# Optimization experiments

Hardware: AMD Instinct MI355X
Metric: run time of the kernel (lower is better)

Reference implementation:

```python
import jax, jax.numpy as jnp
import numpy as np

B, S, NGB, NG, DIM = 64, 4096, 13, 48, 3
NCH = [8, 8, 1]
NSHELLS = 8


def setup_inputs() -> dict:
    key = jax.random.key(0)
    ks = jax.random.split(key, 16)
    rng = np.random.default_rng(0)
    # valid row-wise permutations of the N_ngb neighbor slots per group op
    GnnPerms = jnp.asarray(np.argsort(rng.random((NG, NGB)), axis=1), dtype=jnp.int64)
    NNSites = jax.random.randint(ks[0], (NGB, S), 0, S, dtype=jnp.int64)
    SitesToShells = jax.random.randint(ks[1], (S,), 0, NSHELLS, dtype=jnp.int64)
    # block-diagonal (Ng*dim, Ng*dim) cartesian rotation blocks
    blk = rng.normal(size=(NG, DIM, DIM)).astype(np.float32) * 0.5
    gd = np.zeros((NG * DIM, NG * DIM), np.float32)
    for g in range(NG):
        gd[g * DIM:(g + 1) * DIM, g * DIM:(g + 1) * DIM] = blk[g]
    gdiags = jnp.asarray(gd)
    std = 0.2
    return {
        "InStates": jax.random.normal(ks[2], (B, 1, S), jnp.float32),
        "Psi0": jax.random.normal(ks[3], (NCH[0], 1, NGB), jnp.float32) * std,
        "bias0": jax.random.normal(ks[4], (NCH[0], 1), jnp.float32) * std,
        "Psi1": jax.random.normal(ks[5], (NCH[1], NCH[0], NGB), jnp.float32) * std,
        "bias1": jax.random.normal(ks[6], (NCH[1], 1), jnp.float32) * std,
        "Psi2": jax.random.normal(ks[7], (NCH[2], NCH[1], NGB), jnp.float32) * std,
        "bias2": jax.random.normal(ks[8], (NCH[2], 1), jnp.float32) * std,
        "wtVC": jax.random.normal(ks[9], (DIM, NGB), jnp.float32) * std,
        "ShellWeights": jax.random.normal(ks[10], (NSHELLS,), jnp.float32) * std,
        "gdiags": gdiags,
        "GnnPerms": GnnPerms,
        "NNSites": NNSites,
        "SitesToShells": SitesToShells,
    }


def _rearrange(x, NNSites):
    # x: (B, Nch, S) -> (B, Nch*N_ngb, S); subchannel j of channel c holds x[b, c, NNSites[j, s]]
    b, c, s = x.shape
    return x[:, :, NNSites].reshape(b, c * NGB, s)


def _gconv(x, W, b):
    # x: (B, NchIn*N_ngb, S); W: (NchOut, NchIn, N_ngb); b: (NchOut, 1)
    # group-rotated weights: GW[o, g, c*N_ngb+j] = W[o, c, GnnPerms[g, j]]
    GW = _gconv.GW_cache  # set per-call below via closure-free pattern; replaced in reference
    raise NotImplementedError


def reference(InStates, Psi0, bias0, Psi1, bias1, Psi2, bias2, wtVC,
              ShellWeights, gdiags, GnnPerms, NNSites, SitesToShells):
    act = jax.nn.softplus

    def gconv(x, W, b):
        # rotated weights: (NchOut, Ng, NchIn*N_ngb)
        GW = W[:, :, GnnPerms].transpose(0, 2, 1, 3).reshape(W.shape[0], NG, -1)
        h = jnp.einsum('ogk,bks->bogs', GW, x) + b[:, :, None]  # (B, NchOut, Ng, S)
        return act(h).mean(axis=2)                               # group-orbit average

    out = _rearrange(InStates, NNSites)
    for W, b in ((Psi0, bias0), (Psi1, bias1), (Psi2, bias2)):
        out = gconv(out, W, b)                 # (B, NchOut, S)
        out = _rearrange(out, NNSites)         # (B, NchOut*N_ngb, S)
    # vector channel: row g*dim+d of P is wtVC[d, GnnPerms[g]]
    P = wtVC[:, GnnPerms].transpose(1, 0, 2).reshape(NG * DIM, NGB)
    Wvc = gdiags @ P                           # (Ng*dim, N_ngb)
    v = jnp.einsum('kn,bns->bks', Wvc, out)    # (B, Ng*dim, S)
    v = v.reshape(-1, NG, DIM, out.shape[-1]).mean(axis=1)  # (B, dim, S)
    v = v * ShellWeights[SitesToShells]        # per-site shell weighting
    return v.sum(axis=2) / out.shape[-1]       # (B, dim)
```

## Files before the change

### kernel.cpp

```cpp
#include <hip/hip_runtime.h>
#include <hip/hip_bf16.h>

#define BATCH 64
#define SITES 4096
#define NGB 13
#define NGRP 48
#define SDIM 3

typedef __bf16 bf16x8 __attribute__((ext_vector_type(8)));
typedef float  f32x4  __attribute__((ext_vector_type(4)));

#define OFF_AVC  0
#define OFF_U    64
#define OFF_A0   67648
#define OFF_A1   2164800
#define OFF_PART 4261952
#define UW0H 0
#define UW0L 12288
#define UW1H 24576
#define UW1L 73728
#define UW2H 122880
#define UW2L 129024

__device__ __forceinline__ float softplus_f(float h) {
    return fmaxf(h, 0.f) + __logf(1.f + __expf(-fabsf(h)));
}

__global__ __launch_bounds__(256) void precompute_kernel(
    const float* __restrict__ Psi0, const float* __restrict__ Psi1,
    const float* __restrict__ Psi2, const float* __restrict__ wtVC,
    const float* __restrict__ gdiags, const int* __restrict__ perms,
    float* __restrict__ ws)
{
    float*  Avc = ws + OFF_AVC;
    __bf16* U   = (__bf16*)(ws + OFF_U);
    int t = blockIdx.x * 256 + threadIdx.x;
    if (t < 12288) {
        int k = t & 31, row = t >> 5;
        int o = row / NGRP, g = row - o * NGRP;
        float w = (k < NGB) ? Psi0[o * NGB + perms[g * NGB + k]] : 0.f;
        __bf16 hi = (__bf16)w;
        U[UW0H + t] = hi;
        U[UW0L + t] = (__bf16)(w - (float)hi);
    } else if (t < 61440) {
        int u = t - 12288;
        int k = u & 127, row = u >> 7;
        int o = row / NGRP, g = row - o * NGRP;
        float w = 0.f;
        if (k < 104) { int j = k >> 3, c = k & 7;
                       w = Psi1[(o * 8 + c) * NGB + perms[g * NGB + j]]; }
        __bf16 hi = (__bf16)w;
        U[UW1H + u] = hi;
        U[UW1L + u] = (__bf16)(w - (float)hi);
    } else if (t < 67584) {
        int u = t - 61440;
        int k = u & 127, g = u >> 7;
        float w = 0.f;
        if (k < 104) { int j = k >> 3, c = k & 7;
                       w = Psi2[c * NGB + perms[g * NGB + j]]; }
        __bf16 hi = (__bf16)w;
        U[UW2H + u] = hi;
        U[UW2L + u] = (__bf16)(w - (float)hi);
    } else if (t < 67584 + 39 * NGRP) {
        int t2 = t - 67584;
        int g = t2 % NGRP, u = t2 / NGRP;
        int d = u / NGB, n = u % NGB;
        const int row = g * SDIM + d;
        float s = 0.f;
        for (int k = 0; k < NGRP * SDIM; k++) {
            int g2 = k / SDIM, d2 = k - g2 * SDIM;
            float p = wtVC[d2 * NGB + perms[g2 * NGB + n]];
            s = fmaf(gdiags[row * (NGRP * SDIM) + k], p, s);
        }
        atomicAdd(&Avc[u], s * (1.f / 48.f));
    }
}

template<int NCIN, int NCTOT, int CT, int KPAD, int KSTR, int NWAVES, int NWN,
         int CHUNKS>
__global__ __launch_bounds__(NWAVES * 64) void layer_mfma(
    const float* __restrict__ prev,
    const __bf16* __restrict__ Wh,
    const __bf16* __restrict__ Wl,
    const float* __restrict__ bias,
    const int*   __restrict__ NN,
    float* __restrict__ out)
{
    constexpr int NTHR   = NWAVES * 64;
    constexpr int M      = NCTOT * NGRP;
    constexpr int MTILES = M / 16, NTILES = CT / 16;
    constexpr int NWM    = NWAVES / NWN;
    constexpr int MT_W   = MTILES / NWM, NT_W = NTILES / NWN;
    constexpr int KT     = KPAD / 32;
    constexpr int GS     = NGB * CT;
    constexpr int SPT    = (GS + NTHR - 1) / NTHR;
    constexpr int CPB    = SITES / CT;
    constexpr int BUF    = CT * KSTR;
    constexpr int BPB    = CPB / CHUNKS;

    static_assert(MT_W * 16 == NGRP, "wave covers exactly one o");
    static_assert(NWM * MT_W == MTILES && NWN * NT_W == NTILES, "");
    static_assert((KPAD & 31) == 0 && (KSTR & 7) == 0, "");
    static_assert(CPB % CHUNKS == 0, "block stays within one batch");

    __shared__ __bf16 xh_lds[2 * BUF];
    __shared__ __bf16 xl_lds[2 * BUF];

    const int tid  = threadIdx.x;
    const int wave = tid >> 6, lane = tid & 63;
    const int m16  = lane & 15, quad = lane >> 4;

    const int bid    = blockIdx.x;
    const int b      = bid / BPB;
    const int octet  = bid % BPB;
    const int s0base = octet * (CHUNKS * CT);

    int sj[SPT], scol[SPT];
    bool sv[SPT];
#pragma unroll
    for (int i = 0; i < SPT; i++) {
        int site = tid + i * NTHR;
        sv[i] = (site < GS);
        int ss = sv[i] ? site : 0;
        sj[i] = ss / CT;
        scol[i] = ss % CT;
    }

    auto stage_site = [&](int i, int nn, __bf16* dh, __bf16* dl) {
        if constexpr (NCIN == 1) {
            float v = prev[(size_t)b * SITES + nn];
            __bf16 hi = (__bf16)v;
            dh[scol[i] * KSTR + sj[i]] = hi;
            dl[scol[i] * KSTR + sj[i]] = (__bf16)(v - (float)hi);
        } else {
            const float4* p4 = (const float4*)(prev + ((size_t)(b * SITES + nn)) * 8);
            float4 u0 = p4[0], u1 = p4[1];
            float v[8] = {u0.x, u0.y, u0.z, u0.w, u1.x, u1.y, u1.z, u1.w};
            bf16x8 hv, lv;
#pragma unroll
            for (int c8 = 0; c8 < 8; c8++) {
                __bf16 hi = (__bf16)v[c8];
                hv[c8] = hi;
                lv[c8] = (__bf16)(v[c8] - (float)hi);
            }
            *(bf16x8*)(dh + scol[i] * KSTR + sj[i] * 8) = hv;
            *(bf16x8*)(dl + scol[i] * KSTR + sj[i] * 8) = lv;
        }
    };

    if constexpr (NCIN == 1) {
        for (int e = tid; e < 2 * CT * (KPAD - NGB); e += NTHR) {
            int buf = e / (CT * (KPAD - NGB));
            int r   = e % (CT * (KPAD - NGB));
            int col = r / (KPAD - NGB), p = r % (KPAD - NGB);
            xh_lds[buf * BUF + col * KSTR + NGB + p] = (__bf16)0.f;
            xl_lds[buf * BUF + col * KSTR + NGB + p] = (__bf16)0.f;
        }
    } else {
        const bf16x8 z8 = {};
        for (int e = tid; e < 2 * CT * 3; e += NTHR) {
            int buf = e / (CT * 3);
            int r   = e % (CT * 3);
            int col = r % CT, z = r / CT;
            *(bf16x8*)(xh_lds + buf * BUF + col * KSTR + 104 + z * 8) = z8;
            *(bf16x8*)(xl_lds + buf * BUF + col * KSTR + 104 + z * 8) = z8;
        }
    }

#pragma unroll
    for (int i = 0; i < SPT; i++) if (sv[i]) {
        int nn = NN[sj[i] * SITES + s0base + scol[i]];
        stage_site(i, nn, xh_lds, xl_lds);
    }
    int nnA[SPT];
    if (CHUNKS > 1) {
        const int s1 = s0base + CT;
#pragma unroll
        for (int i = 0; i < SPT; i++)
            nnA[i] = sv[i] ? NN[sj[i] * SITES + s1 + scol[i]] : 0;
    }
    __syncthreads();

    const int wave_mt0 = (wave / NWN) * MT_W;
    const int wave_nt0 = (wave % NWN) * NT_W;
    const int o_g      = (wave_mt0 * 16) / NGRP;
    const float bo     = bias[o_g];

#pragma unroll 1
    for (int c = 0; c < CHUNKS; c++) {
        const int cur = c & 1;
        const __bf16* xh = xh_lds + cur * BUF;
        const __bf16* xl = xl_lds + cur * BUF;

        f32x4 acc[MT_W][NT_W];
#pragma unroll
        for (int mt = 0; mt < MT_W; mt++)
#pragma unroll
            for (int nt = 0; nt < NT_W; nt++) acc[mt][nt] = (f32x4){0.f, 0.f, 0.f, 0.f};

#pragma unroll
        for (int kt = 0; kt < KT; kt++) {
            const int koff = kt * 32 + quad * 8;
            bf16x8 ah[MT_W], al[MT_W], bh[NT_W], bl[NT_W];
#pragma unroll
            for (int mt = 0; mt < MT_W; mt++) {
                int row = (wave_mt0 + mt) * 16 + m16;
                ah[mt] = *(const bf16x8*)(Wh + (size_t)row * KPAD + koff);
                al[mt] = *(const bf16x8*)(Wl + (size_t)row * KPAD + koff);
            }
#pragma unroll
            for (int nt = 0; nt < NT_W; nt++) {
                int cbase = ((wave_nt0 + nt) * 16 + m16) * KSTR + koff;
                bh[nt] = *(const bf16x8*)(xh + cbase);
                bl[nt] = *(const bf16x8*)(xl + cbase);
            }
#pragma unroll
            for (int mt = 0; mt < MT_W; mt++)
#pragma unroll
                for (int nt = 0; nt < NT_W; nt++)
                    acc[mt][nt] = __builtin_amdgcn_mfma_f32_16x16x32_bf16(
                        ah[mt], bh[nt], acc[mt][nt], 0, 0, 0);
#pragma unroll
            for (int mt = 0; mt < MT_W; mt++)
#pragma unroll
                for (int nt = 0; nt < NT_W; nt++)
                    acc[mt][nt] = __builtin_amdgcn_mfma_f32_16x16x32_bf16(
                        al[mt], bh[nt], acc[mt][nt], 0, 0, 0);
#pragma unroll
            for (int mt = 0; mt < MT_W; mt++)
#pragma unroll
                for (int nt = 0; nt < NT_W; nt++)
                    acc[mt][nt] = __builtin_amdgcn_mfma_f32_16x16x32_bf16(
                        ah[mt], bl[nt], acc[mt][nt], 0, 0, 0);
        }

        const int s0c = s0base + c * CT;
#pragma unroll
        for (int nt = 0; nt < NT_W; nt++) {
            float s = 0.f;
#pragma unroll
            for (int mt = 0; mt < MT_W; mt++)
#pragma unroll
                for (int r = 0; r < 4; r++)
                    s += softplus_f(acc[mt][nt][r] + bo);
            s += __shfl_xor(s, 16);
            s += __shfl_xor(s, 32);
            if (quad == 0)
                out[((size_t)(b * SITES + s0c + (wave_nt0 + nt) * 16 + m16)) * NCTOT + o_g]
                    = s * (1.f / 48.f);
        }

        if (c + 1 < CHUNKS) {
            __bf16* dh = xh_lds + (cur ^ 1) * BUF;
            __bf16* dl = xl_lds + (cur ^ 1) * BUF;
#pragma unroll
            for (int i = 0; i < SPT; i++) if (sv[i])
                stage_site(i, nnA[i], dh, dl);
            if (c + 2 < CHUNKS) {
                const int s2 = s0base + (c + 2) * CT;
#pragma unroll
                for (int i = 0; i < SPT; i++)
                    nnA[i] = sv[i] ? NN[sj[i] * SITES + s2 + scol[i]] : 0;
            }
        }
        __syncthreads();
    }
}

__global__ __launch_bounds__(256) void reduce_a(
    const float* __restrict__ A2, const int* __restrict__ NN,
    const int* __restrict__ s2sh, const float* __restrict__ sw,
    const float* __restrict__ Avc, float* __restrict__ partial)
{
    const int b = blockIdx.x >> 4;
    const int chunk = blockIdx.x & 15;
    const int tid = threadIdx.x;
    const int s = (chunk << 8) + tid;
    const float* a = A2 + (size_t)b * SITES;

    float y0 = 0.f, y1 = 0.f, y2 = 0.f;
#pragma unroll
    for (int n = 0; n < NGB; n++) {
        float v = a[NN[n * SITES + s]];
        y0 = fmaf(Avc[n],           v, y0);
        y1 = fmaf(Avc[NGB + n],     v, y1);
        y2 = fmaf(Avc[2 * NGB + n], v, y2);
    }
    const float wgt = sw[s2sh[s]];
    y0 *= wgt; y1 *= wgt; y2 *= wgt;

    __shared__ float red[3][256];
    red[0][tid] = y0; red[1][tid] = y1; red[2][tid] = y2;
    __syncthreads();
    for (int st = 128; st > 0; st >>= 1) {
        if (tid < st) {
            red[0][tid] += red[0][tid + st];
            red[1][tid] += red[1][tid + st];
            red[2][tid] += red[2][tid + st];
        }
        __syncthreads();
    }
    if (tid < 3) partial[(b * 16 + chunk) * 3 + tid] = red[tid][0];
}

__global__ __launch_bounds__(256) void reduce_b(
    const float* __restrict__ partial, float* __restrict__ out)
{
    int t = threadIdx.x;
    if (t < BATCH * 3) {
        int b = t / 3, d = t - b * 3;
        float s = 0.f;
        for (int c = 0; c < 16; c++) s += partial[(b * 16 + c) * 3 + d];
        out[t] = s * (1.f / (float)SITES);
    }
}

extern "C" void kernel_launch(void* const* d_in, const int* in_sizes, int n_in,
                              void* d_out, int out_size, void* d_ws, size_t ws_size,
                              hipStream_t stream)
{
    const float* InStates = (const float*)d_in[0];
    const float* Psi0     = (const float*)d_in[1];
    const float* bias0    = (const float*)d_in[2];
    const float* Psi1     = (const float*)d_in[3];
    const float* bias1    = (const float*)d_in[4];
    const float* Psi2     = (const float*)d_in[5];
    const float* bias2    = (const float*)d_in[6];
    const float* wtVC     = (const float*)d_in[7];
    const float* ShellW   = (const float*)d_in[8];
    const float* gdiags   = (const float*)d_in[9];
    const int*   GnnPerms = (const int*)d_in[10];
    const int*   NNSites  = (const int*)d_in[11];
    const int*   S2Sh     = (const int*)d_in[12];

    float*  ws   = (float*)d_ws;
    float*  Avc  = ws + OFF_AVC;
    __bf16* U    = (__bf16*)(ws + OFF_U);
    float*  A0   = ws + OFF_A0;
    float*  A1   = ws + OFF_A1;
    float*  A2   = ws + OFF_A0;
    float*  PART = ws + OFF_PART;

    float* out = (float*)d_out;

    hipMemsetAsync(Avc, 0, 64 * sizeof(float), stream);
    precompute_kernel<<<272, 256, 0, stream>>>(Psi0, Psi1, Psi2, wtVC, gdiags,
                                               GnnPerms, ws);

    constexpr int CHUNKS = 8;
    constexpr int NBLK   = BATCH * (SITES / 64) / CHUNKS;

    layer_mfma<1, 8, 64, 32, 40, 8, 1, CHUNKS><<<NBLK, 512, 0, stream>>>(
        InStates, U + UW0H, U + UW0L, bias0, NNSites, A0);
    layer_mfma<8, 8, 64, 128, 136, 8, 1, CHUNKS><<<NBLK, 512, 0, stream>>>(
        A0, U + UW1H, U + UW1L, bias1, NNSites, A1);
    layer_mfma<8, 1, 64, 128, 136, 4, 4, CHUNKS><<<NBLK, 256, 0, stream>>>(
        A1, U + UW2H, U + UW2L, bias2, NNSites, A2);

    reduce_a<<<BATCH * 16, 256, 0, stream>>>(A2, NNSites, S2Sh, ShellW, Avc, PART);
    reduce_b<<<1, 256, 0, stream>>>(PART, out);
}
```

Measured before the change: 331.5 us.

## Store intermediate activations as bf16 hi/lo pairs and stage gathers via direct-to-LDS loads

```diff
diff --git a/kernel.cpp b/kernel.cpp
--- a/kernel.cpp
+++ b/kernel.cpp
@@ -12,8 +12,10 @@
 
 #define OFF_AVC  0
 #define OFF_U    64
-#define OFF_A0   67648
-#define OFF_A1   2164800
+#define OFF_A0H  67648
+#define OFF_A0L  1116224
+#define OFF_A1H  2164800
+#define OFF_A1L  3213376
 #define OFF_PART 4261952
 #define UW0H 0
 #define UW0L 12288
@@ -24,6 +26,13 @@
 
 __device__ __forceinline__ float softplus_f(float h) {
     return fmaxf(h, 0.f) + __logf(1.f + __expf(-fabsf(h)));
+}
+
+__device__ __forceinline__ void gld_lds16(const __bf16* g, __bf16* l) {
+    __builtin_amdgcn_global_load_lds(
+        (const __attribute__((address_space(1))) void*)g,
+        (__attribute__((address_space(3))) void*)l,
+        16, 0, 0);
 }
 
 __global__ __launch_bounds__(256) void precompute_kernel(
@@ -76,15 +85,19 @@
     }
 }
 
-template<int NCIN, int NCTOT, int CT, int KPAD, int KSTR, int NWAVES, int NWN,
-         int CHUNKS>
+template<int NCIN, int NCTOT, int OUTF32, int CT, int KPAD, int KSTR,
+         int NWAVES, int NWN, int CHUNKS>
 __global__ __launch_bounds__(NWAVES * 64) void layer_mfma(
-    const float* __restrict__ prev,
+    const float*  __restrict__ prevF,
+    const __bf16* __restrict__ prevH,
+    const __bf16* __restrict__ prevL,
     const __bf16* __restrict__ Wh,
     const __bf16* __restrict__ Wl,
-    const float* __restrict__ bias,
-    const int*   __restrict__ NN,
-    float* __restrict__ out)
+    const float*  __restrict__ bias,
+    const int*    __restrict__ NN,
+    float*  __restrict__ outF,
+    __bf16* __restrict__ outH,
+    __bf16* __restrict__ outL)
 {
     constexpr int NTHR   = NWAVES * 64;
     constexpr int M      = NCTOT * NGRP;
@@ -92,16 +105,17 @@
     constexpr int NWM    = NWAVES / NWN;
     constexpr int MT_W   = MTILES / NWM, NT_W = NTILES / NWN;
     constexpr int KT     = KPAD / 32;
+    constexpr int CPB    = SITES / CT;
+    constexpr int BPB    = CPB / CHUNKS;
+    constexpr int BUF    = (NCIN == 1) ? CT * KSTR : 16 * CT * 8;
     constexpr int GS     = NGB * CT;
     constexpr int SPT    = (GS + NTHR - 1) / NTHR;
-    constexpr int CPB    = SITES / CT;
-    constexpr int BUF    = CT * KSTR;
-    constexpr int BPB    = CPB / CHUNKS;
+    constexpr int JPW    = (NGB + NWAVES - 1) / NWAVES;
 
     static_assert(MT_W * 16 == NGRP, "wave covers exactly one o");
     static_assert(NWM * MT_W == MTILES && NWN * NT_W == NTILES, "");
-    static_assert((KPAD & 31) == 0 && (KSTR & 7) == 0, "");
     static_assert(CPB % CHUNKS == 0, "block stays within one batch");
+    static_assert(NCIN == 1 || CT == 64, "DMA staging: lane==col");
 
     __shared__ __bf16 xh_lds[2 * BUF];
     __shared__ __bf16 xl_lds[2 * BUF];
@@ -125,27 +139,11 @@
         sj[i] = ss / CT;
         scol[i] = ss % CT;
     }
-
-    auto stage_site = [&](int i, int nn, __bf16* dh, __bf16* dl) {
-        if constexpr (NCIN == 1) {
-            float v = prev[(size_t)b * SITES + nn];
-            __bf16 hi = (__bf16)v;
-            dh[scol[i] * KSTR + sj[i]] = hi;
-            dl[scol[i] * KSTR + sj[i]] = (__bf16)(v - (float)hi);
-        } else {
-            const float4* p4 = (const float4*)(prev + ((size_t)(b * SITES + nn)) * 8);
-            float4 u0 = p4[0], u1 = p4[1];
-            float v[8] = {u0.x, u0.y, u0.z, u0.w, u1.x, u1.y, u1.z, u1.w};
-            bf16x8 hv, lv;
-#pragma unroll
-            for (int c8 = 0; c8 < 8; c8++) {
-                __bf16 hi = (__bf16)v[c8];
-                hv[c8] = hi;
-                lv[c8] = (__bf16)(v[c8] - (float)hi);
-            }
-            *(bf16x8*)(dh + scol[i] * KSTR + sj[i] * 8) = hv;
-            *(bf16x8*)(dl + scol[i] * KSTR + sj[i] * 8) = lv;
-        }
+    auto stage_site1 = [&](int i, int nn, __bf16* dh, __bf16* dl) {
+        float v = prevF[(size_t)b * SITES + nn];
+        __bf16 hi = (__bf16)v;
+        dh[scol[i] * KSTR + sj[i]] = hi;
+        dl[scol[i] * KSTR + sj[i]] = (__bf16)(v - (float)hi);
     };
 
     if constexpr (NCIN == 1) {
@@ -158,26 +156,44 @@
         }
     } else {
         const bf16x8 z8 = {};
-        for (int e = tid; e < 2 * CT * 3; e += NTHR) {
-            int buf = e / (CT * 3);
-            int r   = e % (CT * 3);
-            int col = r % CT, z = r / CT;
-            *(bf16x8*)(xh_lds + buf * BUF + col * KSTR + 104 + z * 8) = z8;
-            *(bf16x8*)(xl_lds + buf * BUF + col * KSTR + 104 + z * 8) = z8;
-        }
-    }
-
-#pragma unroll
-    for (int i = 0; i < SPT; i++) if (sv[i]) {
-        int nn = NN[sj[i] * SITES + s0base + scol[i]];
-        stage_site(i, nn, xh_lds, xl_lds);
-    }
+        for (int e = tid; e < 2 * 3 * CT; e += NTHR) {
+            int buf = e / (3 * CT), r = e % (3 * CT);
+            *(bf16x8*)(xh_lds + buf * BUF + (13 * CT + r) * 8) = z8;
+            *(bf16x8*)(xl_lds + buf * BUF + (13 * CT + r) * 8) = z8;
+        }
+    }
+
     int nnA[SPT];
-    if (CHUNKS > 1) {
-        const int s1 = s0base + CT;
-#pragma unroll
-        for (int i = 0; i < SPT; i++)
-            nnA[i] = sv[i] ? NN[sj[i] * SITES + s1 + scol[i]] : 0;
+    int nnP[JPW];
+    if constexpr (NCIN == 1) {
+#pragma unroll
+        for (int i = 0; i < SPT; i++) if (sv[i]) {
+            int nn = NN[sj[i] * SITES + s0base + scol[i]];
+            stage_site1(i, nn, xh_lds, xl_lds);
+        }
+        if (CHUNKS > 1) {
+            const int s1 = s0base + CT;
+#pragma unroll
+            for (int i = 0; i < SPT; i++)
+                nnA[i] = sv[i] ? NN[sj[i] * SITES + s1 + scol[i]] : 0;
+        }
+    } else {
+#pragma unroll
+        for (int u = 0; u < JPW; u++) {
+            int jj = wave + u * NWAVES;
+            if (jj < NGB) {
+                int nn0 = NN[jj * SITES + s0base + lane];
+                gld_lds16(prevH + ((size_t)(b * SITES + nn0)) * 8, xh_lds + jj * CT * 8);
+                gld_lds16(prevL + ((size_t)(b * SITES + nn0)) * 8, xl_lds + jj * CT * 8);
+            }
+        }
+        if (CHUNKS > 1) {
+#pragma unroll
+            for (int u = 0; u < JPW; u++) {
+                int jj = wave + u * NWAVES;
+                nnP[u] = (jj < NGB) ? NN[jj * SITES + s0base + CT + lane] : 0;
+            }
+        }
     }
     __syncthreads();
 
@@ -189,6 +205,30 @@
 #pragma unroll 1
     for (int c = 0; c < CHUNKS; c++) {
         const int cur = c & 1;
+
+        if constexpr (NCIN == 8) {
+            if (c + 1 < CHUNKS) {
+                __bf16* dh = xh_lds + (cur ^ 1) * BUF;
+                __bf16* dl = xl_lds + (cur ^ 1) * BUF;
+#pragma unroll
+                for (int u = 0; u < JPW; u++) {
+                    int jj = wave + u * NWAVES;
+                    if (jj < NGB) {
+                        gld_lds16(prevH + ((size_t)(b * SITES + nnP[u])) * 8, dh + jj * CT * 8);
+                        gld_lds16(prevL + ((size_t)(b * SITES + nnP[u])) * 8, dl + jj * CT * 8);
+                    }
+                }
+                if (c + 2 < CHUNKS) {
+                    const int s2 = s0base + (c + 2) * CT;
+#pragma unroll
+                    for (int u = 0; u < JPW; u++) {
+                        int jj = wave + u * NWAVES;
+                        nnP[u] = (jj < NGB) ? NN[jj * SITES + s2 + lane] : 0;
+                    }
+                }
+            }
+        }
+
         const __bf16* xh = xh_lds + cur * BUF;
         const __bf16* xl = xl_lds + cur * BUF;
 
@@ -210,7 +250,11 @@
             }
 #pragma unroll
             for (int nt = 0; nt < NT_W; nt++) {
-                int cbase = ((wave_nt0 + nt) * 16 + m16) * KSTR + koff;
+                int cbase;
+                if constexpr (NCIN == 1)
+                    cbase = ((wave_nt0 + nt) * 16 + m16) * KSTR + koff;
+                else
+                    cbase = ((kt * 4 + quad) * CT + (wave_nt0 + nt) * 16 + m16) * 8;
                 bh[nt] = *(const bf16x8*)(xh + cbase);
                 bl[nt] = *(const bf16x8*)(xl + cbase);
             }
@@ -245,22 +289,32 @@
                     s += softplus_f(acc[mt][nt][r] + bo);
             s += __shfl_xor(s, 16);
             s += __shfl_xor(s, 32);
-            if (quad == 0)
-                out[((size_t)(b * SITES + s0c + (wave_nt0 + nt) * 16 + m16)) * NCTOT + o_g]
-                    = s * (1.f / 48.f);
-        }
-
-        if (c + 1 < CHUNKS) {
-            __bf16* dh = xh_lds + (cur ^ 1) * BUF;
-            __bf16* dl = xl_lds + (cur ^ 1) * BUF;
-#pragma unroll
-            for (int i = 0; i < SPT; i++) if (sv[i])
-                stage_site(i, nnA[i], dh, dl);
-            if (c + 2 < CHUNKS) {
-                const int s2 = s0base + (c + 2) * CT;
-#pragma unroll
-                for (int i = 0; i < SPT; i++)
-                    nnA[i] = sv[i] ? NN[sj[i] * SITES + s2 + scol[i]] : 0;
+            if (quad == 0) {
+                float sv2 = s * (1.f / 48.f);
+                size_t idx = (size_t)(b * SITES + s0c + (wave_nt0 + nt) * 16 + m16);
+                if constexpr (OUTF32) {
+                    outF[idx] = sv2;
+                } else {
+                    __bf16 hi = (__bf16)sv2;
+                    outH[idx * NCTOT + o_g] = hi;
+                    outL[idx * NCTOT + o_g] = (__bf16)(sv2 - (float)hi);
+                }
+            }
+        }
+
+        if constexpr (NCIN == 1) {
+            if (c + 1 < CHUNKS) {
+                __bf16* dh = xh_lds + (cur ^ 1) * BUF;
+                __bf16* dl = xl_lds + (cur ^ 1) * BUF;
+#pragma unroll
+                for (int i = 0; i < SPT; i++) if (sv[i])
+                    stage_site1(i, nnA[i], dh, dl);
+                if (c + 2 < CHUNKS) {
+                    const int s2 = s0base + (c + 2) * CT;
+#pragma unroll
+                    for (int i = 0; i < SPT; i++)
+                        nnA[i] = sv[i] ? NN[sj[i] * SITES + s2 + scol[i]] : 0;
+                }
             }
         }
         __syncthreads();
@@ -336,9 +390,11 @@
     float*  ws   = (float*)d_ws;
     float*  Avc  = ws + OFF_AVC;
     __bf16* U    = (__bf16*)(ws + OFF_U);
-    float*  A0   = ws + OFF_A0;
-    float*  A1   = ws + OFF_A1;
-    float*  A2   = ws + OFF_A0;
+    __bf16* A0H  = (__bf16*)(ws + OFF_A0H);
+    __bf16* A0L  = (__bf16*)(ws + OFF_A0L);
+    __bf16* A1H  = (__bf16*)(ws + OFF_A1H);
+    __bf16* A1L  = (__bf16*)(ws + OFF_A1L);
+    float*  A2   = ws + OFF_A0H;
     float*  PART = ws + OFF_PART;
 
     float* out = (float*)d_out;
@@ -350,12 +406,15 @@
     constexpr int CHUNKS = 8;
     constexpr int NBLK   = BATCH * (SITES / 64) / CHUNKS;
 
-    layer_mfma<1, 8, 64, 32, 40, 8, 1, CHUNKS><<<NBLK, 512, 0, stream>>>(
-        InStates, U + UW0H, U + UW0L, bias0, NNSites, A0);
-    layer_mfma<8, 8, 64, 128, 136, 8, 1, CHUNKS><<<NBLK, 512, 0, stream>>>(
-        A0, U + UW1H, U + UW1L, bias1, NNSites, A1);
-    layer_mfma<8, 1, 64, 128, 136, 4, 4, CHUNKS><<<NBLK, 256, 0, stream>>>(
-        A1, U + UW2H, U + UW2L, bias2, NNSites, A2);
+    layer_mfma<1, 8, 0, 64, 32, 40, 8, 1, CHUNKS><<<NBLK, 512, 0, stream>>>(
+        InStates, nullptr, nullptr, U + UW0H, U + UW0L, bias0, NNSites,
+        nullptr, A0H, A0L);
+    layer_mfma<8, 8, 0, 64, 128, 136, 8, 1, CHUNKS><<<NBLK, 512, 0, stream>>>(
+        nullptr, A0H, A0L, U + UW1H, U + UW1L, bias1, NNSites,
+        nullptr, A1H, A1L);
+    layer_mfma<8, 1, 1, 64, 128, 136, 4, 4, CHUNKS><<<NBLK, 256, 0, stream>>>(
+        nullptr, A1H, A1L, U + UW2H, U + UW2L, bias2, NNSites,
+        A2, nullptr, nullptr);
 
     reduce_a<<<BATCH * 16, 256, 0, stream>>>(A2, NNSites, S2Sh, ShellW, Avc, PART);
     reduce_b<<<1, 256, 0, stream>>>(PART, out);
```

Result: slower. 360.9 us (+8.9%).

## Interleave next-chunk gather loads and LDS writes with MFMA k-loop

Applied to the files above, without the earlier changes.

```diff
diff --git a/kernel.cpp b/kernel.cpp
--- a/kernel.cpp
+++ b/kernel.cpp
@@ -97,6 +97,8 @@
     constexpr int CPB    = SITES / CT;
     constexpr int BUF    = CT * KSTR;
     constexpr int BPB    = CPB / CHUNKS;
+    constexpr int LKT    = (KT >= 2) ? KT / 2 : 1;
+    constexpr int SPW    = (SPT + LKT - 1) / LKT;
 
     static_assert(MT_W * 16 == NGRP, "wave covers exactly one o");
     static_assert(NWM * MT_W == MTILES && NWN * NT_W == NTILES, "");
@@ -126,26 +128,32 @@
         scol[i] = ss % CT;
     }
 
-    auto stage_site = [&](int i, int nn, __bf16* dh, __bf16* dl) {
-        if constexpr (NCIN == 1) {
-            float v = prev[(size_t)b * SITES + nn];
-            __bf16 hi = (__bf16)v;
-            dh[scol[i] * KSTR + sj[i]] = hi;
-            dl[scol[i] * KSTR + sj[i]] = (__bf16)(v - (float)hi);
-        } else {
-            const float4* p4 = (const float4*)(prev + ((size_t)(b * SITES + nn)) * 8);
-            float4 u0 = p4[0], u1 = p4[1];
-            float v[8] = {u0.x, u0.y, u0.z, u0.w, u1.x, u1.y, u1.z, u1.w};
-            bf16x8 hv, lv;
-#pragma unroll
-            for (int c8 = 0; c8 < 8; c8++) {
-                __bf16 hi = (__bf16)v[c8];
-                hv[c8] = hi;
-                lv[c8] = (__bf16)(v[c8] - (float)hi);
-            }
-            *(bf16x8*)(dh + scol[i] * KSTR + sj[i] * 8) = hv;
-            *(bf16x8*)(dl + scol[i] * KSTR + sj[i] * 8) = lv;
-        }
+    float4 ga[SPT], gb[SPT];
+    float  g1[SPT];
+
+    auto ld8 = [&](int i, int nn) {
+        const float4* p4 = (const float4*)(prev + ((size_t)(b * SITES + nn)) * 8);
+        ga[i] = p4[0];
+        gb[i] = p4[1];
+    };
+    auto wr8 = [&](int i, __bf16* dh, __bf16* dl) {
+        float v[8] = {ga[i].x, ga[i].y, ga[i].z, ga[i].w,
+                      gb[i].x, gb[i].y, gb[i].z, gb[i].w};
+        bf16x8 hv, lv;
+#pragma unroll
+        for (int c8 = 0; c8 < 8; c8++) {
+            __bf16 hi = (__bf16)v[c8];
+            hv[c8] = hi;
+            lv[c8] = (__bf16)(v[c8] - (float)hi);
+        }
+        *(bf16x8*)(dh + scol[i] * KSTR + sj[i] * 8) = hv;
+        *(bf16x8*)(dl + scol[i] * KSTR + sj[i] * 8) = lv;
+    };
+    auto stage_site1 = [&](int i, int nn, __bf16* dh, __bf16* dl) {
+        float v = prev[(size_t)b * SITES + nn];
+        __bf16 hi = (__bf16)v;
+        dh[scol[i] * KSTR + sj[i]] = hi;
+        dl[scol[i] * KSTR + sj[i]] = (__bf16)(v - (float)hi);
     };
 
     if constexpr (NCIN == 1) {
@@ -167,12 +175,17 @@
         }
     }
 
+    int nnA[SPT];
 #pragma unroll
     for (int i = 0; i < SPT; i++) if (sv[i]) {
         int nn = NN[sj[i] * SITES + s0base + scol[i]];
-        stage_site(i, nn, xh_lds, xl_lds);
-    }
-    int nnA[SPT];
+        if constexpr (NCIN == 1) {
+            stage_site1(i, nn, xh_lds, xl_lds);
+        } else {
+            ld8(i, nn);
+            wr8(i, xh_lds, xl_lds);
+        }
+    }
     if (CHUNKS > 1) {
         const int s1 = s0base + CT;
 #pragma unroll
@@ -191,6 +204,9 @@
         const int cur = c & 1;
         const __bf16* xh = xh_lds + cur * BUF;
         const __bf16* xl = xl_lds + cur * BUF;
+        __bf16* dh = xh_lds + (cur ^ 1) * BUF;
+        __bf16* dl = xl_lds + (cur ^ 1) * BUF;
+        const bool do_stage = (c + 1 < CHUNKS);
 
         f32x4 acc[MT_W][NT_W];
 #pragma unroll
@@ -232,6 +248,34 @@
                 for (int nt = 0; nt < NT_W; nt++)
                     acc[mt][nt] = __builtin_amdgcn_mfma_f32_16x16x32_bf16(
                         ah[mt], bl[nt], acc[mt][nt], 0, 0, 0);
+
+            if constexpr (NCIN == 8 && KT >= 2) {
+                if (do_stage) {
+                    if (kt < LKT) {
+#pragma unroll
+                        for (int u = 0; u < SPW; u++) {
+                            constexpr int dummy = 0; (void)dummy;
+                            int i = kt * SPW + u;
+                            if (i < SPT && sv[i]) ld8(i, nnA[i]);
+                        }
+                    } else {
+#pragma unroll
+                        for (int u = 0; u < SPW; u++) {
+                            int i = (kt - LKT) * SPW + u;
+                            if (i < SPT && sv[i]) wr8(i, dh, dl);
+                        }
+                    }
+                }
+            }
+        }
+
+        if constexpr (NCIN == 8) {
+            if (c + 2 < CHUNKS) {
+                const int s2 = s0base + (c + 2) * CT;
+#pragma unroll
+                for (int i = 0; i < SPT; i++)
+                    nnA[i] = sv[i] ? NN[sj[i] * SITES + s2 + scol[i]] : 0;
+            }
         }
 
         const int s0c = s0base + c * CT;
@@ -250,17 +294,17 @@
                     = s * (1.f / 48.f);
         }
 
-        if (c + 1 < CHUNKS) {
-            __bf16* dh = xh_lds + (cur ^ 1) * BUF;
-            __bf16* dl = xl_lds + (cur ^ 1) * BUF;
-#pragma unroll
-            for (int i = 0; i < SPT; i++) if (sv[i])
-                stage_site(i, nnA[i], dh, dl);
-            if (c + 2 < CHUNKS) {
-                const int s2 = s0base + (c + 2) * CT;
-#pragma unroll
-                for (int i = 0; i < SPT; i++)
-                    nnA[i] = sv[i] ? NN[sj[i] * SITES + s2 + scol[i]] : 0;
+        if constexpr (NCIN == 1) {
+            if (do_stage) {
+#pragma unroll
+                for (int i = 0; i < SPT; i++) if (sv[i])
+                    stage_site1(i, nnA[i], dh, dl);
+                if (c + 2 < CHUNKS) {
+                    const int s2 = s0base + (c + 2) * CT;
+#pragma unroll
+                    for (int i = 0; i < SPT; i++)
+                        nnA[i] = sv[i] ? NN[sj[i] * SITES + s2 + scol[i]] : 0;
+                }
             }
         }
         __syncthreads();
```

Result: no change. 331.7 us (+0.1%).

## Replace MFMA for the first and last layers with fp32 VALU kernels

Applied to the files above, without the earlier changes.

```diff
diff --git a/kernel.cpp b/kernel.cpp
--- a/kernel.cpp
+++ b/kernel.cpp
@@ -11,16 +11,14 @@
 typedef float  f32x4  __attribute__((ext_vector_type(4)));
 
 #define OFF_AVC  0
+#define OFF_GW0F 64
+#define OFF_GW2F 5056
 #define OFF_U    64
 #define OFF_A0   67648
 #define OFF_A1   2164800
 #define OFF_PART 4261952
-#define UW0H 0
-#define UW0L 12288
 #define UW1H 24576
 #define UW1L 73728
-#define UW2H 122880
-#define UW2L 129024
 
 __device__ __forceinline__ float softplus_f(float h) {
     return fmaxf(h, 0.f) + __logf(1.f + __expf(-fabsf(h)));
@@ -32,18 +30,22 @@
     const float* __restrict__ gdiags, const int* __restrict__ perms,
     float* __restrict__ ws)
 {
-    float*  Avc = ws + OFF_AVC;
-    __bf16* U   = (__bf16*)(ws + OFF_U);
+    float*  Avc  = ws + OFF_AVC;
+    float*  GW0F = ws + OFF_GW0F;
+    float*  GW2F = ws + OFF_GW2F;
+    __bf16* U    = (__bf16*)(ws + OFF_U);
     int t = blockIdx.x * 256 + threadIdx.x;
-    if (t < 12288) {
-        int k = t & 31, row = t >> 5;
-        int o = row / NGRP, g = row - o * NGRP;
-        float w = (k < NGB) ? Psi0[o * NGB + perms[g * NGB + k]] : 0.f;
-        __bf16 hi = (__bf16)w;
-        U[UW0H + t] = hi;
-        U[UW0L + t] = (__bf16)(w - (float)hi);
-    } else if (t < 61440) {
-        int u = t - 12288;
+    if (t < 4992) {
+        int g = t / 104, r = t % 104;
+        int o = r / NGB, j = r % NGB;
+        GW0F[t] = Psi0[o * NGB + perms[g * NGB + j]];
+    } else if (t < 9984) {
+        int u = t - 4992;
+        int g = u / 104, k = u % 104;
+        int j = k >> 3, c = k & 7;
+        GW2F[u] = Psi2[c * NGB + perms[g * NGB + j]];
+    } else if (t < 9984 + 49152) {
+        int u = t - 9984;
         int k = u & 127, row = u >> 7;
         int o = row / NGRP, g = row - o * NGRP;
         float w = 0.f;
@@ -52,17 +54,8 @@
         __bf16 hi = (__bf16)w;
         U[UW1H + u] = hi;
         U[UW1L + u] = (__bf16)(w - (float)hi);
-    } else if (t < 67584) {
-        int u = t - 61440;
-        int k = u & 127, g = u >> 7;
-        float w = 0.f;
-        if (k < 104) { int j = k >> 3, c = k & 7;
-                       w = Psi2[c * NGB + perms[g * NGB + j]]; }
-        __bf16 hi = (__bf16)w;
-        U[UW2H + u] = hi;
-        U[UW2L + u] = (__bf16)(w - (float)hi);
-    } else if (t < 67584 + 39 * NGRP) {
-        int t2 = t - 67584;
+    } else if (t < 59136 + 39 * NGRP) {
+        int t2 = t - 59136;
         int g = t2 % NGRP, u = t2 / NGRP;
         int d = u / NGB, n = u % NGB;
         const int row = g * SDIM + d;
@@ -74,6 +67,94 @@
         }
         atomicAdd(&Avc[u], s * (1.f / 48.f));
     }
+}
+
+__global__ __launch_bounds__(256) void l0_valu(
+    const float* __restrict__ In,
+    const float* __restrict__ GW0F,
+    const float* __restrict__ bias0,
+    const int*   __restrict__ NN,
+    float* __restrict__ A0)
+{
+    const int b = blockIdx.x >> 4;
+    const int s = ((blockIdx.x & 15) << 8) + threadIdx.x;
+    const float* row = In + (size_t)b * SITES;
+
+    int nn[NGB];
+#pragma unroll
+    for (int j = 0; j < NGB; j++) nn[j] = NN[j * SITES + s];
+    float x[NGB];
+#pragma unroll
+    for (int j = 0; j < NGB; j++) x[j] = row[nn[j]];
+
+    float bo[8];
+#pragma unroll
+    for (int o = 0; o < 8; o++) bo[o] = bias0[o];
+
+    float a[8];
+#pragma unroll
+    for (int o = 0; o < 8; o++) a[o] = 0.f;
+
+#pragma unroll 2
+    for (int g = 0; g < NGRP; g++) {
+        const float* w = GW0F + g * 104;
+        float h[8];
+#pragma unroll
+        for (int o = 0; o < 8; o++) h[o] = bo[o];
+#pragma unroll
+        for (int o = 0; o < 8; o++)
+#pragma unroll
+            for (int j = 0; j < NGB; j++)
+                h[o] = fmaf(w[o * NGB + j], x[j], h[o]);
+#pragma unroll
+        for (int o = 0; o < 8; o++) a[o] += softplus_f(h[o]);
+    }
+
+    float* dst = A0 + ((size_t)(b * SITES + s)) * 8;
+    f32x4 v0 = {a[0], a[1], a[2], a[3]};
+    f32x4 v1 = {a[4], a[5], a[6], a[7]};
+    const float k = 1.f / 48.f;
+    v0 *= k; v1 *= k;
+    *(f32x4*)(dst)     = v0;
+    *(f32x4*)(dst + 4) = v1;
+}
+
+__global__ __launch_bounds__(256) void l2_valu(
+    const float* __restrict__ A1,
+    const float* __restrict__ GW2F,
+    const float* __restrict__ bias2,
+    const int*   __restrict__ NN,
+    float* __restrict__ A2)
+{
+    const int b = blockIdx.x >> 4;
+    const int s = ((blockIdx.x & 15) << 8) + threadIdx.x;
+
+    int nn[NGB];
+#pragma unroll
+    for (int j = 0; j < NGB; j++) nn[j] = NN[j * SITES + s];
+
+    const float b2 = bias2[0];
+    float acc[NGRP];
+#pragma unroll
+    for (int g = 0; g < NGRP; g++) acc[g] = b2;
+
+#pragma unroll 2
+    for (int j = 0; j < NGB; j++) {
+        const float4* p = (const float4*)(A1 + ((size_t)(b * SITES + nn[j])) * 8);
+        float4 u0 = p[0], u1 = p[1];
+        float x[8] = {u0.x, u0.y, u0.z, u0.w, u1.x, u1.y, u1.z, u1.w};
+        const float* w = GW2F + j * 8;
+#pragma unroll
+        for (int g = 0; g < NGRP; g++)
+#pragma unroll
+            for (int c = 0; c < 8; c++)
+                acc[g] = fmaf(w[g * 104 + c], x[c], acc[g]);
+    }
+
+    float a = 0.f;
+#pragma unroll
+    for (int g = 0; g < NGRP; g++) a += softplus_f(acc[g]);
+    A2[(size_t)b * SITES + s] = a * (1.f / 48.f);
 }
 
 template<int NCIN, int NCTOT, int CT, int KPAD, int KSTR, int NWAVES, int NWN,
@@ -102,6 +183,7 @@
     static_assert(NWM * MT_W == MTILES && NWN * NT_W == NTILES, "");
     static_assert((KPAD & 31) == 0 && (KSTR & 7) == 0, "");
     static_assert(CPB % CHUNKS == 0, "block stays within one batch");
+    static_assert(NCIN == 8, "v18: only the 8-channel layer uses MFMA");
 
     __shared__ __bf16 xh_lds[2 * BUF];
     __shared__ __bf16 xl_lds[2 * BUF];
@@ -127,36 +209,21 @@
     }
 
     auto stage_site = [&](int i, int nn, __bf16* dh, __bf16* dl) {
-        if constexpr (NCIN == 1) {
-            float v = prev[(size_t)b * SITES + nn];
-            __bf16 hi = (__bf16)v;
-            dh[scol[i] * KSTR + sj[i]] = hi;
-            dl[scol[i] * KSTR + sj[i]] = (__bf16)(v - (float)hi);
-        } else {
-            const float4* p4 = (const float4*)(prev + ((size_t)(b * SITES + nn)) * 8);
-            float4 u0 = p4[0], u1 = p4[1];
-            float v[8] = {u0.x, u0.y, u0.z, u0.w, u1.x, u1.y, u1.z, u1.w};
-            bf16x8 hv, lv;
-#pragma unroll
-            for (int c8 = 0; c8 < 8; c8++) {
-                __bf16 hi = (__bf16)v[c8];
-                hv[c8] = hi;
-                lv[c8] = (__bf16)(v[c8] - (float)hi);
-            }
-            *(bf16x8*)(dh + scol[i] * KSTR + sj[i] * 8) = hv;
-            *(bf16x8*)(dl + scol[i] * KSTR + sj[i] * 8) = lv;
-        }
+        const float4* p4 = (const float4*)(prev + ((size_t)(b * SITES + nn)) * 8);
+        float4 u0 = p4[0], u1 = p4[1];
+        float v[8] = {u0.x, u0.y, u0.z, u0.w, u1.x, u1.y, u1.z, u1.w};
+        bf16x8 hv, lv;
+#pragma unroll
+        for (int c8 = 0; c8 < 8; c8++) {
+            __bf16 hi = (__bf16)v[c8];
+            hv[c8] = hi;
+            lv[c8] = (__bf16)(v[c8] - (float)hi);
+        }
+        *(bf16x8*)(dh + scol[i] * KSTR + sj[i] * 8) = hv;
+        *(bf16x8*)(dl + scol[i] * KSTR + sj[i] * 8) = lv;
     };
 
-    if constexpr (NCIN == 1) {
-        for (int e = tid; e < 2 * CT * (KPAD - NGB); e += NTHR) {
-            int buf = e / (CT * (KPAD - NGB));
-            int r   = e % (CT * (KPAD - NGB));
-            int col = r / (KPAD - NGB), p = r % (KPAD - NGB);
-            xh_lds[buf * BUF + col * KSTR + NGB + p] = (__bf16)0.f;
-            xl_lds[buf * BUF + col * KSTR + NGB + p] = (__bf16)0.f;
-        }
-    } else {
+    {
         const bf16x8 z8 = {};
         for (int e = tid; e < 2 * CT * 3; e += NTHR) {
             int buf = e / (CT * 3);
@@ -167,12 +234,12 @@
         }
     }
 
+    int nnA[SPT];
 #pragma unroll
     for (int i = 0; i < SPT; i++) if (sv[i]) {
         int nn = NN[sj[i] * SITES + s0base + scol[i]];
         stage_site(i, nn, xh_lds, xl_lds);
     }
-    int nnA[SPT];
     if (CHUNKS > 1) {
         const int s1 = s0base + CT;
 #pragma unroll
@@ -335,6 +402,8 @@
 
     float*  ws   = (float*)d_ws;
     float*  Avc  = ws + OFF_AVC;
+    float*  GW0F = ws + OFF_GW0F;
+    float*  GW2F = ws + OFF_GW2F;
     __bf16* U    = (__bf16*)(ws + OFF_U);
     float*  A0   = ws + OFF_A0;
     float*  A1   = ws + OFF_A1;
@@ -344,18 +413,16 @@
     float* out = (float*)d_out;
 
     hipMemsetAsync(Avc, 0, 64 * sizeof(float), stream);
-    precompute_kernel<<<272, 256, 0, stream>>>(Psi0, Psi1, Psi2, wtVC, gdiags,
+    precompute_kernel<<<239, 256, 0, stream>>>(Psi0, Psi1, Psi2, wtVC, gdiags,
                                                GnnPerms, ws);
 
     constexpr int CHUNKS = 8;
     constexpr int NBLK   = BATCH * (SITES / 64) / CHUNKS;
 
-    layer_mfma<1, 8, 64, 32, 40, 8, 1, CHUNKS><<<NBLK, 512, 0, stream>>>(
-        InStates, U + UW0H, U + UW0L, bias0, NNSites, A0);
+    l0_valu<<<BATCH * 16, 256, 0, stream>>>(InStates, GW0F, bias0, NNSites, A0);
     layer_mfma<8, 8, 64, 128, 136, 8, 1, CHUNKS><<<NBLK, 512, 0, stream>>>(
         A0, U + UW1H, U + UW1L, bias1, NNSites, A1);
-    layer_mfma<8, 1, 64, 128, 136, 4, 4, CHUNKS><<<NBLK, 256, 0, stream>>>(
-        A1, U + UW2H, U + UW2L, bias2, NNSites, A2);
+    l2_valu<<<BATCH * 16, 256, 0, stream>>>(A1, GW2F, bias2, NNSites, A2);
 
     reduce_a<<<BATCH * 16, 256, 0, stream>>>(A2, NNSites, S2Sh, ShellW, Avc, PART);
     reduce_b<<<1, 256, 0, stream>>>(PART, out);
```

New measurement: 380.7 us. +14.9%, slower.
